# Performance work log

Measured on AMD Instinct MI355X. Metric: run time of the kernel, lower is better.

Reference implementation:

```python
import jax, jax.numpy as jnp
import numpy as np

H = 4096          # hidden_size
NH = 32           # num_attention_heads
NKV = 2           # multi_query_group_num (kv heads)
HD = 128          # kv_channels / head_dim
RD = 64           # rotary_dim = head_dim * rotary_percent(0.5)
T = 2048          # total tokens (single prefill sequence)
EPS = 1e-5        # layernorm_epsilon
ROPE_BASE = 10000.0


def setup_inputs() -> dict:
    key = jax.random.key(0)
    k0, k1, k2, k3 = jax.random.split(key, 4)
    qkv_out = (NH + 2 * NKV) * HD  # 4608
    return {
        "positions": jnp.arange(T, dtype=jnp.int32),
        "hidden_states": jax.random.normal(k0, (T, H), jnp.float32),
        "w_qkv": jax.random.normal(k1, (qkv_out, H), jnp.float32) * 0.02,
        "b_qkv": jax.random.normal(k2, (qkv_out,), jnp.float32) * 0.02,
        "w_dense": jax.random.normal(k3, (H, NH * HD), jnp.float32) * 0.02,
        "q_ln_w": jnp.ones((HD,), jnp.float32),
        "k_ln_w": jnp.ones((HD,), jnp.float32),
    }


def _rmsnorm(x, w):
    # per-head RMSNorm over head_dim
    return x * jax.lax.rsqrt(jnp.mean(x * x, axis=-1, keepdims=True) + EPS) * w


def _rope(x, positions):
    # partial rotary (first RD dims), interleaved GPT-J style (is_neox_style=False)
    inv_freq = 1.0 / (ROPE_BASE ** (jnp.arange(0, RD, 2, dtype=jnp.float32) / RD))
    ang = positions.astype(jnp.float32)[:, None] * inv_freq      # [T, RD//2]
    cos = jnp.cos(ang)[:, None, :]                               # [T, 1, RD//2]
    sin = jnp.sin(ang)[:, None, :]
    x_rot, x_pass = x[..., :RD], x[..., RD:]
    x1 = x_rot[..., 0::2]
    x2 = x_rot[..., 1::2]
    r1 = x1 * cos - x2 * sin
    r2 = x2 * cos + x1 * sin
    x_rot = jnp.stack([r1, r2], axis=-1).reshape(x.shape[:-1] + (RD,))
    return jnp.concatenate([x_rot, x_pass], axis=-1)


def reference(positions, hidden_states, w_qkv, b_qkv, w_dense, q_ln_w, k_ln_w):
    qkv = hidden_states @ w_qkv.T + b_qkv                        # [T, 4608]
    q_size, kv_size = NH * HD, NKV * HD
    q = qkv[:, :q_size].reshape(T, NH, HD)
    k = qkv[:, q_size:q_size + kv_size].reshape(T, NKV, HD)
    v = qkv[:, q_size + kv_size:].reshape(T, NKV, HD)
    # optional qk layernorm (RMSNorm since config.rmsnorm)
    q = _rmsnorm(q, q_ln_w)
    k = _rmsnorm(k, k_ln_w)
    # rotary embedding
    q = _rope(q, positions)
    k = _rope(k, positions)
    # GQA: expand kv heads to query heads
    group = NH // NKV
    k_exp = jnp.repeat(k, group, axis=1)                         # [T, NH, HD]
    v_exp = jnp.repeat(v, group, axis=1)
    scale = HD ** -0.5
    scores = jnp.einsum("thd,shd->hts", q, k_exp) * scale        # [NH, T, T]
    causal = jnp.tril(jnp.ones((T, T), dtype=bool))
    scores = jnp.where(causal[None, :, :], scores, jnp.finfo(scores.dtype).min)
    attn = jax.nn.softmax(scores, axis=-1)
    out = jnp.einsum("hts,shd->thd", attn, v_exp).reshape(T, NH * HD)
    return out @ w_dense.T                                       # [T, H]
```

## Files before the change

kernel.cpp:

```cpp
#include <hip/hip_runtime.h>
#include <cstdint>
#include <cstddef>

typedef short short4v __attribute__((ext_vector_type(4)));
typedef short short8v __attribute__((ext_vector_type(8)));
typedef float f32x4   __attribute__((ext_vector_type(4)));

#define T_LEN  2048
#define HDIM   4096
#define NHEADS 32
#define HEADD  128
#define QKVN   4608

static __device__ __forceinline__ short f2bf(float f) {
  __bf16 h = (__bf16)f;
  return __builtin_bit_cast(short, h);
}
static __device__ __forceinline__ float bf2f(short u) {
  return __builtin_bit_cast(float, ((unsigned int)(unsigned short)u) << 16);
}

static __device__ __forceinline__ void gload_lds16(const void* g, void* l) {
  __builtin_amdgcn_global_load_lds((const __attribute__((address_space(1))) void*)g,
                                   (__attribute__((address_space(3))) void*)l,
                                   16, 0, 0);
}

__global__ void cast_f32_to_bf16(const float* __restrict__ in, short* __restrict__ out, int n4) {
  int idx = blockIdx.x * blockDim.x + threadIdx.x;
  int stride = gridDim.x * blockDim.x;
  const float4* in4 = (const float4*)in;
  short4v* out4 = (short4v*)out;
  for (int i = idx; i < n4; i += stride) {
    float4 v = in4[i];
    short4v o;
    o[0] = f2bf(v.x); o[1] = f2bf(v.y); o[2] = f2bf(v.z); o[3] = f2bf(v.w);
    out4[i] = o;
  }
}

template <int OUT_BF16>
__global__ __launch_bounds__(256, 2) void gemm_bt(
    const short* __restrict__ A,
    const short* __restrict__ B,
    const float* __restrict__ bias,
    void* __restrict__ Cout,
    int M, int N, int K)
{
  __shared__ short sA[128 * 32];
  __shared__ short sB[128 * 32];
  const int tid  = threadIdx.x;
  const int lane = tid & 63;
  const int wv   = tid >> 6;
  const int wr   = wv >> 1;
  const int wc   = wv & 1;
  const int bn0  = blockIdx.x * 128;
  const int bm0  = blockIdx.y * 128;

  const int row0 = tid >> 2;
  const int kc0  = (tid & 3) * 8;
  const int row1 = row0 + 64;
  short* lA0 = sA + wv * 64 * 8;
  short* lA1 = sA + (256 + wv * 64) * 8;
  short* lB0 = sB + wv * 64 * 8;
  short* lB1 = sB + (256 + wv * 64) * 8;
  const short* gA0 = A + (size_t)(bm0 + row0) * K + kc0;
  const short* gA1 = A + (size_t)(bm0 + row1) * K + kc0;
  const short* gB0 = B + (size_t)(bn0 + row0) * K + kc0;
  const short* gB1 = B + (size_t)(bn0 + row1) * K + kc0;

  const int fr = lane & 15;
  const int fk = (lane >> 4) * 8;

  f32x4 zero = {0.f, 0.f, 0.f, 0.f};
  f32x4 acc[4][4];
#pragma unroll
  for (int m = 0; m < 4; m++)
#pragma unroll
    for (int n = 0; n < 4; n++) acc[m][n] = zero;

  for (int kt = 0; kt < K; kt += 32) {
    gload_lds16(gA0 + kt, lA0);
    gload_lds16(gA1 + kt, lA1);
    gload_lds16(gB0 + kt, lB0);
    gload_lds16(gB1 + kt, lB1);
    __syncthreads();
    short8v af[4], bfr[4];
#pragma unroll
    for (int m = 0; m < 4; m++)
      af[m] = *(const short8v*)(sA + (wr * 64 + m * 16 + fr) * 32 + fk);
#pragma unroll
    for (int n = 0; n < 4; n++)
      bfr[n] = *(const short8v*)(sB + (wc * 64 + n * 16 + fr) * 32 + fk);
#pragma unroll
    for (int m = 0; m < 4; m++)
#pragma unroll
      for (int n = 0; n < 4; n++)
        acc[m][n] = __builtin_amdgcn_mfma_f32_16x16x32_bf16(af[m], bfr[n], acc[m][n], 0, 0, 0);
    __syncthreads();
  }

  const int rg = (lane >> 4) * 4;
#pragma unroll
  for (int m = 0; m < 4; m++) {
#pragma unroll
    for (int n = 0; n < 4; n++) {
      const int gcol = bn0 + wc * 64 + n * 16 + fr;
      const float bv = bias ? bias[gcol] : 0.0f;
#pragma unroll
      for (int j = 0; j < 4; j++) {
        const int grow = bm0 + wr * 64 + m * 16 + rg + j;
        const float v = acc[m][n][j] + bv;
        if (OUT_BF16)
          ((short*)Cout)[(size_t)grow * N + gcol] = f2bf(v);
        else
          ((float*)Cout)[(size_t)grow * N + gcol] = v;
      }
    }
  }
}

__global__ __launch_bounds__(64) void qkv_post_kernel(
    const short* __restrict__ qkvb,
    const int*   __restrict__ positions,
    const float* __restrict__ q_ln,
    const float* __restrict__ k_ln,
    short* __restrict__ Qb,
    short* __restrict__ Kb,
    short* __restrict__ Vt)
{
  const int t = blockIdx.x;
  const int h = blockIdx.y;
  const int lane = threadIdx.x;
  const unsigned int pk =
      ((const unsigned int*)(qkvb + (size_t)t * QKVN + h * HEADD))[lane];
  float x = bf2f((short)(pk & 0xffffu));
  float y = bf2f((short)(pk >> 16));

  if (h >= 34) {
    const int hv = h - 34;
    short* dst = Vt + ((size_t)hv * HEADD + 2 * lane) * T_LEN + t;
    dst[0]     = f2bf(x);
    dst[T_LEN] = f2bf(y);
    return;
  }

  float ss = x * x + y * y;
#pragma unroll
  for (int d = 32; d > 0; d >>= 1) ss += __shfl_xor(ss, d);
  const float r = rsqrtf(ss * (1.0f / 128.0f) + 1e-5f);
  const float* lnw = (h < 32) ? q_ln : k_ln;
  x = x * r * lnw[2 * lane];
  y = y * r * lnw[2 * lane + 1];

  if (lane < 32) {
    const float pos = (float)positions[t];
    const float ang = pos * powf(10000.0f, -(float)lane * (1.0f / 32.0f));
    const float c = cosf(ang), s = sinf(ang);
    const float r1 = x * c - y * s;
    const float r2 = y * c + x * s;
    x = r1; y = r2;
  }

  short* dst = (h < 32) ? (Qb + ((size_t)h * T_LEN + t) * HEADD + 2 * lane)
                        : (Kb + ((size_t)(h - 32) * T_LEN + t) * HEADD + 2 * lane);
  dst[0] = f2bf(x);
  dst[1] = f2bf(y);
}

__global__ __launch_bounds__(256, 2) void attn_kernel(
    const short* __restrict__ Qb,
    const short* __restrict__ Kb,
    const short* __restrict__ Vt,
    short* __restrict__ attn_out)
{
  __shared__ short Ks[2][64 * 128];
  __shared__ short Vs[2][128 * 64];
  __shared__ short pbuf[4][32 * 64];
  const int blk  = gridDim.x - 1 - blockIdx.x;
  const int h    = blockIdx.y;
  const int hkv  = h >> 4;
  const int tid  = threadIdx.x;
  const int lane = tid & 63;
  const int wv   = tid >> 6;
  const int B0   = blk * 128;
  const int qrow0 = B0 + wv * 32;
  const int fr = lane & 15;
  const int fk = (lane >> 4) * 8;
  const int fkb = (lane >> 4) << 4;
  const int rg = (lane >> 4) * 4;
  const int swz = (fr & 7) << 4;

  const short* Kh = Kb + (size_t)hkv * T_LEN * HEADD;
  const short* Vh = Vt + (size_t)hkv * HEADD * T_LEN;

  short8v qf[2][4];
#pragma unroll
  for (int g = 0; g < 2; g++) {
    const short* Qrow = Qb + ((size_t)h * T_LEN + qrow0 + g * 16 + fr) * HEADD + fk;
#pragma unroll
    for (int d0 = 0; d0 < 4; d0++) qf[g][d0] = *(const short8v*)(Qrow + d0 * 32);
  }

  float mrow[2][4], lrow[2][4];
#pragma unroll
  for (int g = 0; g < 2; g++)
#pragma unroll
    for (int j = 0; j < 4; j++) { mrow[g][j] = -1e30f; lrow[g][j] = 0.f; }
  f32x4 zero = {0.f, 0.f, 0.f, 0.f};
  f32x4 o[2][8];
#pragma unroll
  for (int g = 0; g < 2; g++)
#pragma unroll
    for (int d = 0; d < 8; d++) o[g][d] = zero;

  char* pb = (char*)&pbuf[wv][0];
  const float scale = 0.08838834764831845f;
  const int nt = 2 * blk + 2;

  auto STAGE = [&](int b, int t) {
    const int s0 = t * 64;
#pragma unroll
    for (int i = 0; i < 4; i++) {
      const int c    = i * 256 + tid;
      const int row  = c >> 4;
      const int colb = (c & 15) << 4;
      const int scol = (colb ^ ((row & 7) << 4)) >> 1;
      gload_lds16(Kh + (size_t)(s0 + row) * HEADD + scol,
                  (char*)&Ks[b][0] + (size_t)(i * 256 + wv * 64) * 16);
    }
#pragma unroll
    for (int i = 0; i < 4; i++) {
      const int c    = i * 256 + tid;
      const int row  = c >> 3;
      const int colb = (c & 7) << 4;
      const int scol = (colb ^ ((row & 7) << 4)) >> 1;
      gload_lds16(Vh + (size_t)row * T_LEN + s0 + scol,
                  (char*)&Vs[b][0] + (size_t)(i * 256 + wv * 64) * 16);
    }
  };

  int cur = 0;
  STAGE(0, 0);
  __syncthreads();

  for (int t = 0; t < nt; ++t) {
    if (t + 1 < nt) STAGE(cur ^ 1, t + 1);
    const int s0 = t * 64;
    const char* KsB = (const char*)&Ks[cur][0];
    const char* VsB = (const char*)&Vs[cur][0];

    float scv[2][4][4];
#pragma unroll
    for (int sub = 0; sub < 4; sub++) {
      const char* Kbase = KsB + (sub * 16 + fr) * 256;
      f32x4 a0 = zero, a1 = zero;
#pragma unroll
      for (int d0 = 0; d0 < 4; d0++) {
        short8v kf = *(const short8v*)(Kbase + ((d0 * 64 + fkb) ^ swz));
        a0 = __builtin_amdgcn_mfma_f32_16x16x32_bf16(qf[0][d0], kf, a0, 0, 0, 0);
        a1 = __builtin_amdgcn_mfma_f32_16x16x32_bf16(qf[1][d0], kf, a1, 0, 0, 0);
      }
#pragma unroll
      for (int j = 0; j < 4; j++) {
        scv[0][sub][j] = a0[j] * scale;
        scv[1][sub][j] = a1[j] * scale;
      }
    }
    if (t >= nt - 2) {
#pragma unroll
      for (int g = 0; g < 2; g++)
#pragma unroll
        for (int sub = 0; sub < 4; sub++) {
          const int colp = s0 + sub * 16 + fr;
#pragma unroll
          for (int j = 0; j < 4; j++)
            if (colp > qrow0 + g * 16 + rg + j) scv[g][sub][j] = -1e30f;
        }
    }
    float pmax[2][4];
#pragma unroll
    for (int g = 0; g < 2; g++)
#pragma unroll
      for (int j = 0; j < 4; j++)
        pmax[g][j] = fmaxf(fmaxf(scv[g][0][j], scv[g][1][j]),
                           fmaxf(scv[g][2][j], scv[g][3][j]));
    float growth = -1e30f;
#pragma unroll
    for (int g = 0; g < 2; g++)
#pragma unroll
      for (int j = 0; j < 4; j++) growth = fmaxf(growth, pmax[g][j] - mrow[g][j]);
    if (!__all(growth <= 8.0f)) {
#pragma unroll
      for (int g = 0; g < 2; g++)
#pragma unroll
        for (int j = 0; j < 4; j++) {
          float mx = pmax[g][j];
#pragma unroll
          for (int d = 1; d < 16; d <<= 1) mx = fmaxf(mx, __shfl_xor(mx, d));
          const float mn = fmaxf(mrow[g][j], mx);
          const float c  = __expf(mrow[g][j] - mn);
          mrow[g][j] = mn;
          lrow[g][j] *= c;
#pragma unroll
          for (int df = 0; df < 8; df++) o[g][df][j] *= c;
        }
    }
#pragma unroll
    for (int g = 0; g < 2; g++)
#pragma unroll
      for (int j = 0; j < 4; j++) {
        const int prow = g * 16 + rg + j;
        char* prb = pb + prow * 128;
        const int rswz = ((rg + j) & 7) << 4;
        float ps = 0.f;
#pragma unroll
        for (int sub = 0; sub < 4; sub++) {
          const float p = __expf(scv[g][sub][j] - mrow[g][j]);
          ps += p;
          *(short*)(prb + ((((sub * 16 + fr) << 1)) ^ rswz)) = f2bf(p);
        }
        lrow[g][j] += ps;
      }
    asm volatile("" ::: "memory");
    short8v pf[2][2];
#pragma unroll
    for (int g = 0; g < 2; g++)
#pragma unroll
      for (int ks = 0; ks < 2; ks++)
        pf[g][ks] = *(const short8v*)(pb + (g * 16 + fr) * 128 + ((ks * 64 + fkb) ^ swz));
#pragma unroll
    for (int df = 0; df < 8; df++) {
      const char* Vbase = VsB + (df * 16 + fr) * 128;
      short8v vf0 = *(const short8v*)(Vbase + ((0 + fkb) ^ swz));
      short8v vf1 = *(const short8v*)(Vbase + ((64 + fkb) ^ swz));
      o[0][df] = __builtin_amdgcn_mfma_f32_16x16x32_bf16(pf[0][0], vf0, o[0][df], 0, 0, 0);
      o[0][df] = __builtin_amdgcn_mfma_f32_16x16x32_bf16(pf[0][1], vf1, o[0][df], 0, 0, 0);
      o[1][df] = __builtin_amdgcn_mfma_f32_16x16x32_bf16(pf[1][0], vf0, o[1][df], 0, 0, 0);
      o[1][df] = __builtin_amdgcn_mfma_f32_16x16x32_bf16(pf[1][1], vf1, o[1][df], 0, 0, 0);
    }
    __syncthreads();
    cur ^= 1;
  }

#pragma unroll
  for (int g = 0; g < 2; g++)
#pragma unroll
    for (int j = 0; j < 4; j++) {
#pragma unroll
      for (int d = 1; d < 16; d <<= 1) lrow[g][j] += __shfl_xor(lrow[g][j], d);
    }
#pragma unroll
  for (int g = 0; g < 2; g++)
#pragma unroll
    for (int df = 0; df < 8; df++)
#pragma unroll
      for (int j = 0; j < 4; j++) {
        const float v = o[g][df][j] / lrow[g][j];
        attn_out[(size_t)(qrow0 + g * 16 + rg + j) * HDIM + h * HEADD + df * 16 + fr] = f2bf(v);
      }
}

extern "C" void kernel_launch(void* const* d_in, const int* in_sizes, int n_in,
                              void* d_out, int out_size, void* d_ws, size_t ws_size,
                              hipStream_t stream) {
  (void)out_size; (void)ws_size;
  int ip = 0, ih = 1, iwq = 2, ib = 3, iwd = 4, il0 = 5, il1 = 6;
  if (n_in == 7) {
    int p = -1, hh = -1, wq = -1, b = -1, wd = -1, l0 = -1, l1 = -1, ok = 1;
    for (int i = 0; i < 7; i++) {
      switch (in_sizes[i]) {
        case 2048:     p  = i; break;
        case 8388608:  hh = i; break;
        case 18874368: wq = i; break;
        case 4608:     b  = i; break;
        case 16777216: wd = i; break;
        case 128:      if (l0 < 0) l0 = i; else l1 = i; break;
        default:       ok = 0; break;
      }
    }
    if (ok && p >= 0 && hh >= 0 && wq >= 0 && b >= 0 && wd >= 0 && l0 >= 0 && l1 >= 0) {
      ip = p; ih = hh; iwq = wq; ib = b; iwd = wd; il0 = l0; il1 = l1;
    }
  }

  const int*   positions = (const int*)d_in[ip];
  const float* hidden    = (const float*)d_in[ih];
  const float* w_qkv     = (const float*)d_in[iwq];
  const float* b_qkv     = (const float*)d_in[ib];
  const float* w_dense   = (const float*)d_in[iwd];
  const float* q_ln      = (const float*)d_in[il0];
  const float* k_ln      = (const float*)d_in[il1];

  char* ws = (char*)d_ws;
  short* Ahs   = (short*)(ws + 0);
  short* Qb    = (short*)(ws + 0);
  short* Wqkv  = (short*)(ws + (size_t)16777216);
  short* Kb    = (short*)(ws + (size_t)16777216);
  short* Vt    = (short*)(ws + (size_t)17825792);
  short* Wd    = (short*)(ws + (size_t)18874368);
  short* qkvb  = (short*)(ws + (size_t)54525952);
  short* attnb = (short*)(ws + (size_t)54525952);

  cast_f32_to_bf16<<<dim3(1024), dim3(256), 0, stream>>>(hidden, Ahs, (T_LEN * HDIM) / 4);
  cast_f32_to_bf16<<<dim3(2048), dim3(256), 0, stream>>>(w_qkv, Wqkv, (QKVN * HDIM) / 4);
  gemm_bt<1><<<dim3(QKVN / 128, T_LEN / 128), dim3(256), 0, stream>>>(
      Ahs, Wqkv, b_qkv, (void*)qkvb, T_LEN, QKVN, HDIM);
  qkv_post_kernel<<<dim3(T_LEN, 36), dim3(64), 0, stream>>>(
      qkvb, positions, q_ln, k_ln, Qb, Kb, Vt);
  cast_f32_to_bf16<<<dim3(2048), dim3(256), 0, stream>>>(w_dense, Wd, (HDIM * HDIM) / 4);
  attn_kernel<<<dim3(16, NHEADS), dim3(256), 0, stream>>>(Qb, Kb, Vt, attnb);
  gemm_bt<0><<<dim3(HDIM / 128, T_LEN / 128), dim3(256), 0, stream>>>(
      attnb, Wd, nullptr, d_out, T_LEN, HDIM, HDIM);
}
```

Baseline: 350.8 us.

## Double-buffer GEMM LDS tiles and remap workgroups across XCDs

Adds a second LDS buffer so the global-to-LDS load of the next K tile is issued before the MFMA work on the current tile, removing one barrier per iteration and overlapping load latency with compute. It also remaps workgroup ids so consecutive blocks spread across the 8 XCDs in column-major tile order, aiming for better L2 reuse. The cost is doubled LDS per block, which may limit occupancy. Correctness relies on the async LDS loads finishing before the single barrier, and the remap assumes the grid size is divisible by 8.

```diff
diff --git a/kernel.cpp b/kernel.cpp
--- a/kernel.cpp
+++ b/kernel.cpp
@@ -47,23 +47,23 @@
     void* __restrict__ Cout,
     int M, int N, int K)
 {
-  __shared__ short sA[128 * 32];
-  __shared__ short sB[128 * 32];
+  __shared__ short sA[2][128 * 32];
+  __shared__ short sB[2][128 * 32];
   const int tid  = threadIdx.x;
   const int lane = tid & 63;
   const int wv   = tid >> 6;
   const int wr   = wv >> 1;
   const int wc   = wv & 1;
-  const int bn0  = blockIdx.x * 128;
-  const int bm0  = blockIdx.y * 128;
+
+  const int nwg  = gridDim.x * gridDim.y;
+  int wgid = blockIdx.y * gridDim.x + blockIdx.x;
+  wgid = (wgid & 7) * (nwg >> 3) + (wgid >> 3);
+  const int bn0 = (wgid / gridDim.y) * 128;
+  const int bm0 = (wgid % gridDim.y) * 128;
 
   const int row0 = tid >> 2;
   const int kc0  = (tid & 3) * 8;
   const int row1 = row0 + 64;
-  short* lA0 = sA + wv * 64 * 8;
-  short* lA1 = sA + (256 + wv * 64) * 8;
-  short* lB0 = sB + wv * 64 * 8;
-  short* lB1 = sB + (256 + wv * 64) * 8;
   const short* gA0 = A + (size_t)(bm0 + row0) * K + kc0;
   const short* gA1 = A + (size_t)(bm0 + row1) * K + kc0;
   const short* gB0 = B + (size_t)(bn0 + row0) * K + kc0;
@@ -72,6 +72,15 @@
   const int fr = lane & 15;
   const int fk = (lane >> 4) * 8;
 
+  auto STAGE = [&](int b, int kt) {
+    short* lA = &sA[b][0] + wv * 64 * 8;
+    short* lB = &sB[b][0] + wv * 64 * 8;
+    gload_lds16(gA0 + kt, lA);
+    gload_lds16(gA1 + kt, lA + 256 * 8);
+    gload_lds16(gB0 + kt, lB);
+    gload_lds16(gB1 + kt, lB + 256 * 8);
+  };
+
   f32x4 zero = {0.f, 0.f, 0.f, 0.f};
   f32x4 acc[4][4];
 #pragma unroll
@@ -79,25 +88,28 @@
 #pragma unroll
     for (int n = 0; n < 4; n++) acc[m][n] = zero;
 
+  int cur = 0;
+  STAGE(0, 0);
+  __syncthreads();
+
   for (int kt = 0; kt < K; kt += 32) {
-    gload_lds16(gA0 + kt, lA0);
-    gload_lds16(gA1 + kt, lA1);
-    gload_lds16(gB0 + kt, lB0);
-    gload_lds16(gB1 + kt, lB1);
-    __syncthreads();
+    if (kt + 32 < K) STAGE(cur ^ 1, kt + 32);
+    const short* aB = &sA[cur][0];
+    const short* bB = &sB[cur][0];
     short8v af[4], bfr[4];
 #pragma unroll
     for (int m = 0; m < 4; m++)
-      af[m] = *(const short8v*)(sA + (wr * 64 + m * 16 + fr) * 32 + fk);
+      af[m] = *(const short8v*)(aB + (wr * 64 + m * 16 + fr) * 32 + fk);
 #pragma unroll
     for (int n = 0; n < 4; n++)
-      bfr[n] = *(const short8v*)(sB + (wc * 64 + n * 16 + fr) * 32 + fk);
+      bfr[n] = *(const short8v*)(bB + (wc * 64 + n * 16 + fr) * 32 + fk);
 #pragma unroll
     for (int m = 0; m < 4; m++)
 #pragma unroll
       for (int n = 0; n < 4; n++)
         acc[m][n] = __builtin_amdgcn_mfma_f32_16x16x32_bf16(af[m], bfr[n], acc[m][n], 0, 0, 0);
     __syncthreads();
+    cur ^= 1;
   }
 
   const int rg = (lane >> 4) * 4;
```

After: 355.6 us. Within noise of the previous version (+1.4%).
